# Optimization experiments

Measured on AMD Instinct MI355X. Metric: run time of the kernel, lower is better.

## Reference

```python
import jax, jax.numpy as jnp
import numpy as np

EMB = 1024
HEADS = 16
HEADSIZE = EMB // HEADS


def _layernorm(x, gamma, beta, eps=1e-5):
    # LayerNorm over the last dim (headsize), affine.
    mu = jnp.mean(x, axis=-1, keepdims=True)
    var = jnp.var(x, axis=-1, keepdims=True)
    return (x - mu) * jax.lax.rsqrt(var + eps) * gamma + beta


def setup_inputs() -> dict:
    key = jax.random.key(0)
    ks = jax.random.split(key, 12)
    B, TI, TC = 4, 1024, 1024
    s = 1.0 / np.sqrt(EMB)
    inp = {
        "x": jax.random.normal(ks[0], (B, TI, EMB), dtype=jnp.float32),
        "context": jax.random.normal(ks[1], (B, TC, EMB), dtype=jnp.float32),
        # torch nn.Linear weights are (out, in); y = x @ W.T
        "Wq": jax.random.uniform(ks[2], (EMB, EMB), jnp.float32, -s, s),
        "Wk": jax.random.uniform(ks[3], (EMB, EMB), jnp.float32, -s, s),
        "Wv": jax.random.uniform(ks[4], (EMB, EMB), jnp.float32, -s, s),
        "Wu": jax.random.uniform(ks[5], (EMB, EMB), jnp.float32, -s, s),
        "bu": jax.random.uniform(ks[6], (EMB,), jnp.float32, -s, s),
        "q_gamma": jnp.ones((HEADSIZE,), jnp.float32),
        "q_beta": jnp.zeros((HEADSIZE,), jnp.float32),
        "k_gamma": jnp.ones((HEADSIZE,), jnp.float32),
        "k_beta": jnp.zeros((HEADSIZE,), jnp.float32),
    }
    return inp


def reference(x, context, Wq, Wk, Wv, Wu, bu, q_gamma, q_beta, k_gamma, k_beta):
    B, TI, E = x.shape
    TC = context.shape[1]
    T = TI + TC
    xc = jnp.concatenate([x, context], axis=1)  # [B, T, E]

    q = (x @ Wq.T).reshape(B, TI, HEADS, HEADSIZE)
    k = (xc @ Wk.T).reshape(B, T, HEADS, HEADSIZE)
    v = (xc @ Wv.T).reshape(B, T, HEADS, HEADSIZE)

    # optional QK-LayerNorm over headsize
    q = _layernorm(q, q_gamma, q_beta)
    k = _layernorm(k, k_gamma, k_beta)

    scale = E ** 0.25
    q = q / scale
    k = k / scale

    # scores: [B, H, TI, T]
    dot = jnp.einsum("bihd,bjhd->bhij", q, k)
    attn = jax.nn.softmax(dot, axis=-1)
    out = jnp.einsum("bhij,bjhd->bihd", attn, v).reshape(B, TI, E)
    return out @ Wu.T + bu
```

## Files before the change

kernel.cpp:

```cpp
#include <hip/hip_runtime.h>
#include <cstdint>


typedef unsigned short u16;
typedef __attribute__((ext_vector_type(8))) short bf16x8;
typedef __attribute__((ext_vector_type(4))) float f32x4;
typedef __attribute__((ext_vector_type(4))) unsigned short u16x4;

#define GLDS(gsrc, ldst)                                                              \
  __builtin_amdgcn_global_load_lds(                                                   \
      (const __attribute__((address_space(1))) unsigned int*)(gsrc),                  \
      (__attribute__((address_space(3))) unsigned int*)(ldst), 16, 0, 0)

__device__ __forceinline__ u16 f2bf(float x) {
  unsigned int u = __float_as_uint(x);
  u += 0x7fffu + ((u >> 16) & 1u);
  return (u16)(u >> 16);
}

__device__ __forceinline__ f32x4 mfma16(bf16x8 a, bf16x8 b, f32x4 c) {
  return __builtin_amdgcn_mfma_f32_16x16x32_bf16(a, b, c, 0, 0, 0);
}


__global__ __launch_bounds__(256) void cast_concat(const float* __restrict__ x,
                                                   const float* __restrict__ c,
                                                   u16* __restrict__ o) {
  const int n4 = (8 << 20) / 4;
  for (int i = blockIdx.x * blockDim.x + threadIdx.x; i < n4; i += gridDim.x * blockDim.x) {
    int elem = i * 4;
    int b = elem >> 21;
    int rem = elem & ((1 << 21) - 1);
    int r = rem >> 10;
    int e = rem & 1023;
    const float* src = (r < 1024) ? (x + ((((size_t)(b << 10)) + r) << 10) + e)
                                  : (c + ((((size_t)(b << 10)) + (r - 1024)) << 10) + e);
    float4 v = *(const float4*)src;
    u16x4 ov;
    ov.x = f2bf(v.x); ov.y = f2bf(v.y); ov.z = f2bf(v.z); ov.w = f2bf(v.w);
    *(u16x4*)(o + elem) = ov;
  }
}

__global__ __launch_bounds__(256) void cast_w(const float* __restrict__ w0,
                                              const float* __restrict__ w1,
                                              const float* __restrict__ w2,
                                              const float* __restrict__ w3,
                                              u16* __restrict__ o) {
  const int n4 = (4 << 20) / 4;
  for (int i = blockIdx.x * blockDim.x + threadIdx.x; i < n4; i += gridDim.x * blockDim.x) {
    int elem = i * 4;
    int sel = elem >> 20;
    int loc = elem & ((1 << 20) - 1);
    const float* s = (sel == 0) ? w0 : (sel == 1) ? w1 : (sel == 2) ? w2 : w3;
    float4 v = *(const float4*)(s + loc);
    u16x4 ov;
    ov.x = f2bf(v.x); ov.y = f2bf(v.y); ov.z = f2bf(v.z); ov.w = f2bf(v.w);
    *(u16x4*)(o + elem) = ov;
  }
}


template <int EPI>
__global__ __launch_bounds__(256)
void gemm_bt(const u16* __restrict__ A, const u16* __restrict__ Bw,
             u16* __restrict__ Ob, float* __restrict__ Of,
             const float* __restrict__ P0, const float* __restrict__ P1,
             int M, int N, int K, int rpbo, int rpbi, float oscale) {
  __shared__ alignas(16) u16 lA[128 * 32];
  __shared__ alignas(16) u16 lB[128 * 32];
  const int tid = threadIdx.x;
  const int wv = tid >> 6, l = tid & 63, g = l >> 4, c16 = l & 15;
  const int wr = wv >> 1, wc = wv & 1;
  const int m0 = blockIdx.x * 128, n0 = blockIdx.y * 128;
  const int arow0 = (m0 / rpbo) * rpbi + (m0 % rpbo);

  f32x4 acc[4][4];
  const f32x4 z4 = {0.f, 0.f, 0.f, 0.f};
#pragma unroll
  for (int i = 0; i < 4; ++i)
#pragma unroll
    for (int j = 0; j < 4; ++j) acc[i][j] = z4;

  const int srow = tid >> 2;
  const int scA = (tid & 3) ^ (srow & 3);
  const u16* aSrc = A + (size_t)(arow0 + srow) * K + scA * 8;
  const u16* bSrc = Bw + (size_t)(n0 + srow) * K + scA * 8;
  char* ldA = (char*)lA;
  char* ldB = (char*)lB;
  const int lof = wv * 1024;

  const int ksteps = K >> 5;
  for (int kt = 0; kt < ksteps; ++kt) {
    const int kof = kt << 5;
    GLDS(aSrc + kof, ldA + lof);
    GLDS(aSrc + (size_t)64 * K + kof, ldA + 4096 + lof);
    GLDS(bSrc + kof, ldB + lof);
    GLDS(bSrc + (size_t)64 * K + kof, ldB + 4096 + lof);
    __syncthreads();
    bf16x8 af[4], bfr[4];
#pragma unroll
    for (int mi = 0; mi < 4; ++mi) {
      int row = wr * 64 + mi * 16 + c16;
      af[mi] = *(const bf16x8*)(ldA + row * 64 + ((g * 16) ^ ((row & 3) << 4)));
    }
#pragma unroll
    for (int ni = 0; ni < 4; ++ni) {
      int row = wc * 64 + ni * 16 + c16;
      bfr[ni] = *(const bf16x8*)(ldB + row * 64 + ((g * 16) ^ ((row & 3) << 4)));
    }
#pragma unroll
    for (int mi = 0; mi < 4; ++mi)
#pragma unroll
      for (int ni = 0; ni < 4; ++ni)
        acc[mi][ni] = mfma16(af[mi], bfr[ni], acc[mi][ni]);
    __syncthreads();
  }

  if constexpr (EPI == 2) {
#pragma unroll
    for (int ni = 0; ni < 4; ++ni) {
      int col = n0 + wc * 64 + ni * 16 + c16;
      float bv = P0[col];
#pragma unroll
      for (int mi = 0; mi < 4; ++mi) {
        int row = m0 + wr * 64 + mi * 16 + g * 4;
        float* dst = Of + (size_t)row * N + col;
#pragma unroll
        for (int r = 0; r < 4; ++r) dst[(size_t)r * N] = acc[mi][ni][r] + bv;
      }
    }
  } else if constexpr (EPI == 1) {
#pragma unroll
    for (int ni = 0; ni < 4; ++ni) {
      int col = n0 + wc * 64 + ni * 16 + c16;
      int hh = col >> 6, dd = col & 63;
#pragma unroll
      for (int mi = 0; mi < 4; ++mi) {
        int m = m0 + wr * 64 + mi * 16 + g * 4;
        int bb = m >> 11, tt = m & 2047;
        u16x4 o;
#pragma unroll
        for (int r = 0; r < 4; ++r) o[r] = f2bf(acc[mi][ni][r]);
        *(u16x4*)(Ob + ((size_t)((bb * 16 + hh) * 64 + dd)) * 2048 + tt) = o;
      }
    }
  } else {
#pragma unroll
    for (int mi = 0; mi < 4; ++mi) {
      float sum[4], sq[4];
#pragma unroll
      for (int r = 0; r < 4; ++r) {
        float s = 0.f, q = 0.f;
#pragma unroll
        for (int ni = 0; ni < 4; ++ni) {
          float v = acc[mi][ni][r];
          s += v;
          q += v * v;
        }
#pragma unroll
        for (int msk = 1; msk < 16; msk <<= 1) {
          s += __shfl_xor(s, msk);
          q += __shfl_xor(q, msk);
        }
        sum[r] = s;
        sq[r] = q;
      }
#pragma unroll
      for (int ni = 0; ni < 4; ++ni) {
        int dloc = ni * 16 + c16;
        int colg = n0 + wc * 64 + ni * 16 + c16;
        float gv = P0[dloc], bv = P1[dloc];
#pragma unroll
        for (int r = 0; r < 4; ++r) {
          float mean = sum[r] * (1.f / 64.f);
          float var = sq[r] * (1.f / 64.f) - mean * mean;
          float y = (acc[mi][ni][r] - mean) * rsqrtf(var + 1e-5f) * gv + bv;
          int row = m0 + wr * 64 + mi * 16 + g * 4 + r;
          Ob[(size_t)row * N + colg] = f2bf(y * oscale);
        }
      }
    }
  }
}


__global__ __launch_bounds__(256)
void attn_kernel(const u16* __restrict__ Q, const u16* __restrict__ Kb,
                 const u16* __restrict__ Vt, u16* __restrict__ AO) {
  __shared__ alignas(16) u16 lK[64 * 64];
  __shared__ alignas(16) u16 lV[64 * 64];
  const int tid = threadIdx.x;
  const int wv = tid >> 6, l = tid & 63, g = l >> 4, c16 = l & 15;
  const int b = blockIdx.z, h = blockIdx.y, qt = blockIdx.x;
  const int qrow = (b << 10) + (qt << 6) + (wv << 4) + c16;

  const u16* qp = Q + (size_t)qrow * 1024 + h * 64 + g * 8;
  bf16x8 qf0 = *(const bf16x8*)(qp);
  bf16x8 qf1 = *(const bf16x8*)(qp + 32);

  const f32x4 z4 = {0.f, 0.f, 0.f, 0.f};
  f32x4 acc_o[4];
#pragma unroll
  for (int i = 0; i < 4; ++i) acc_o[i] = z4;
  float m_run = -3.0e38f, l_run = 0.f;

  const u16* Kbase = Kb + (size_t)(b * 2048) * 1024 + (size_t)h * 64;
  const u16* Vbase = Vt + (size_t)((b * 16 + h) * 64) * 2048;
  const int prow = tid >> 3, pch = tid & 7;
  const int sc = pch ^ (prow & 7);
  const int lof = wv * 1024;

  for (int t32 = 0; t32 < 32; ++t32) {
    const int kv0 = t32 << 6;
    GLDS(Kbase + (size_t)(kv0 + prow) * 1024 + sc * 8, (char*)lK + lof);
    GLDS(Kbase + (size_t)(kv0 + prow + 32) * 1024 + sc * 8, (char*)lK + 4096 + lof);
    GLDS(Vbase + (size_t)prow * 2048 + kv0 + sc * 8, (char*)lV + lof);
    GLDS(Vbase + (size_t)(prow + 32) * 2048 + kv0 + sc * 8, (char*)lV + 4096 + lof);
    __syncthreads();

    f32x4 s[4];
#pragma unroll
    for (int nk = 0; nk < 4; ++nk) s[nk] = z4;
#pragma unroll
    for (int nk = 0; nk < 4; ++nk) {
      int row = nk * 16 + c16;
      int swz = (row & 7) << 4;
      bf16x8 ka0 = *(const bf16x8*)((char*)lK + row * 128 + ((g * 16) ^ swz));
      bf16x8 ka1 = *(const bf16x8*)((char*)lK + row * 128 + ((64 + g * 16) ^ swz));
      s[nk] = mfma16(ka0, qf0, s[nk]);
      s[nk] = mfma16(ka1, qf1, s[nk]);
    }

    float tm = -3.0e38f;
#pragma unroll
    for (int nk = 0; nk < 4; ++nk)
#pragma unroll
      for (int r = 0; r < 4; ++r) tm = fmaxf(tm, s[nk][r]);
    tm = fmaxf(tm, __shfl_xor(tm, 16));
    tm = fmaxf(tm, __shfl_xor(tm, 32));
    float mnew = fmaxf(m_run, tm);
    float corr = __expf(m_run - mnew);
    float ts = 0.f;
#pragma unroll
    for (int nk = 0; nk < 4; ++nk)
#pragma unroll
      for (int r = 0; r < 4; ++r) {
        float p = __expf(s[nk][r] - mnew);
        s[nk][r] = p;
        ts += p;
      }
    ts += __shfl_xor(ts, 16);
    ts += __shfl_xor(ts, 32);
    l_run = l_run * corr + ts;
    m_run = mnew;
#pragma unroll
    for (int nd = 0; nd < 4; ++nd) acc_o[nd] *= corr;

    unsigned int pk[4][2];
#pragma unroll
    for (int nk = 0; nk < 4; ++nk) {
      pk[nk][0] = (unsigned int)f2bf(s[nk][0]) | ((unsigned int)f2bf(s[nk][1]) << 16);
      pk[nk][1] = (unsigned int)f2bf(s[nk][2]) | ((unsigned int)f2bf(s[nk][3]) << 16);
    }

#pragma unroll
    for (int c = 0; c < 2; ++c) {
      union {
        unsigned int w[4];
        bf16x8 v;
      } pb;
#pragma unroll
      for (int wj = 0; wj < 4; ++wj) {
        int srcl = ((l & 16) << 1) + ((wj & 2) << 3) + c16;
        unsigned int lo = (unsigned int)__shfl((int)pk[c * 2][wj & 1], srcl);
        unsigned int hi = (unsigned int)__shfl((int)pk[c * 2 + 1][wj & 1], srcl);
        pb.w[wj] = (l & 32) ? hi : lo;
      }
#pragma unroll
      for (int nd = 0; nd < 4; ++nd) {
        int row = nd * 16 + c16;
        int swz = (row & 7) << 4;
        bf16x8 va = *(const bf16x8*)((char*)lV + row * 128 + (((c << 6) + (g << 4)) ^ swz));
        acc_o[nd] = mfma16(va, pb.v, acc_o[nd]);
      }
    }
    __syncthreads();
  }

  float invl = 1.f / l_run;
#pragma unroll
  for (int nd = 0; nd < 4; ++nd) {
    u16x4 o;
#pragma unroll
    for (int r = 0; r < 4; ++r) o[r] = f2bf(acc_o[nd][r] * invl);
    *(u16x4*)(AO + (size_t)qrow * 1024 + h * 64 + nd * 16 + (g << 2)) = o;
  }
}


extern "C" void kernel_launch(void* const* d_in, const int* in_sizes, int n_in,
                              void* d_out, int out_size, void* d_ws, size_t ws_size,
                              hipStream_t stream) {
  const float* x = (const float*)d_in[0];
  const float* ctx = (const float*)d_in[1];
  const float* Wq = (const float*)d_in[2];
  const float* Wk = (const float*)d_in[3];
  const float* Wv = (const float*)d_in[4];
  const float* Wu = (const float*)d_in[5];
  const float* bu = (const float*)d_in[6];
  const float* qg = (const float*)d_in[7];
  const float* qb = (const float*)d_in[8];
  const float* kg = (const float*)d_in[9];
  const float* kb = (const float*)d_in[10];
  float* out = (float*)d_out;

  char* w = (char*)d_ws;
  u16* XCB = (u16*)(w);
  u16* WQB = (u16*)(w + ((size_t)16 << 20));
  u16* WKB = (u16*)(w + ((size_t)18 << 20));
  u16* WVB = (u16*)(w + ((size_t)20 << 20));
  u16* WUB = (u16*)(w + ((size_t)22 << 20));
  u16* QBB = (u16*)(w + ((size_t)24 << 20));
  u16* KBB = (u16*)(w + ((size_t)32 << 20));
  u16* VT = (u16*)(w + ((size_t)48 << 20));
  u16* AO = (u16*)(w + ((size_t)64 << 20));

  const float invs = 0.17677669529663687f;

  cast_concat<<<2048, 256, 0, stream>>>(x, ctx, XCB);
  cast_w<<<1024, 256, 0, stream>>>(Wq, Wk, Wv, Wu, WQB);

  gemm_bt<0><<<dim3(32, 8), 256, 0, stream>>>(XCB, WQB, QBB, nullptr, qg, qb,
                                              4096, 1024, 1024, 1024, 2048, invs);
  gemm_bt<0><<<dim3(64, 8), 256, 0, stream>>>(XCB, WKB, KBB, nullptr, kg, kb,
                                              8192, 1024, 1024, 2048, 2048, invs);
  gemm_bt<1><<<dim3(64, 8), 256, 0, stream>>>(XCB, WVB, VT, nullptr, nullptr, nullptr,
                                              8192, 1024, 1024, 2048, 2048, 1.f);

  attn_kernel<<<dim3(16, 16, 4), 256, 0, stream>>>(QBB, KBB, VT, AO);

  gemm_bt<2><<<dim3(32, 8), 256, 0, stream>>>(AO, WUB, nullptr, out, bu, nullptr,
                                              4096, 1024, 1024, 4096, 4096, 1.f);
}
```

Before: 305.0 us.

## Double-buffer GEMM and attention tiles, switch attention to 32x32 MFMA with lazy rescale

Adds double-buffered LDS staging to the GEMM and attention loops so the next tile's global-to-LDS load is issued before the current tile is computed. The attention kernel is rewritten around 32x32x16 MFMA with 128 query rows per block (half the grid). It folds log2(e) into the Q scale so exp2f can be used, and skips the running-max rescale unless the max grows by more than 8. It also uses s_setprio around the MFMA sections and drops the LDS swizzle in attention. The costs are doubled LDS use, possible bank conflicts from the unswizzled layout, and the lazy rescale relying on bounded exponent growth for numerical safety.

```diff
diff --git a/kernel.cpp b/kernel.cpp
--- a/kernel.cpp
+++ b/kernel.cpp
@@ -5,6 +5,7 @@
 typedef unsigned short u16;
 typedef __attribute__((ext_vector_type(8))) short bf16x8;
 typedef __attribute__((ext_vector_type(4))) float f32x4;
+typedef __attribute__((ext_vector_type(16))) float f32x16;
 typedef __attribute__((ext_vector_type(4))) unsigned short u16x4;
 
 #define GLDS(gsrc, ldst)                                                              \
@@ -20,6 +21,9 @@
 
 __device__ __forceinline__ f32x4 mfma16(bf16x8 a, bf16x8 b, f32x4 c) {
   return __builtin_amdgcn_mfma_f32_16x16x32_bf16(a, b, c, 0, 0, 0);
+}
+__device__ __forceinline__ f32x16 mfma32(bf16x8 a, bf16x8 b, f32x16 c) {
+  return __builtin_amdgcn_mfma_f32_32x32x16_bf16(a, b, c, 0, 0, 0);
 }
 
 
@@ -67,8 +71,8 @@
              u16* __restrict__ Ob, float* __restrict__ Of,
              const float* __restrict__ P0, const float* __restrict__ P1,
              int M, int N, int K, int rpbo, int rpbi, float oscale) {
-  __shared__ alignas(16) u16 lA[128 * 32];
-  __shared__ alignas(16) u16 lB[128 * 32];
+  __shared__ alignas(16) u16 lA[2][128 * 32];
+  __shared__ alignas(16) u16 lB[2][128 * 32];
   const int tid = threadIdx.x;
   const int wv = tid >> 6, l = tid & 63, g = l >> 4, c16 = l & 15;
   const int wr = wv >> 1, wc = wv & 1;
@@ -91,23 +95,33 @@
   const int lof = wv * 1024;
 
   const int ksteps = K >> 5;
+#define STAGE_G(bi, kof)                                   \
+  {                                                        \
+    char* dA = ldA + (bi)*8192 + lof;                      \
+    char* dB = ldB + (bi)*8192 + lof;                      \
+    GLDS(aSrc + (kof), dA);                                \
+    GLDS(aSrc + (size_t)64 * K + (kof), dA + 4096);        \
+    GLDS(bSrc + (kof), dB);                                \
+    GLDS(bSrc + (size_t)64 * K + (kof), dB + 4096);        \
+  }
+
+  STAGE_G(0, 0);
+  __syncthreads();
+  int buf = 0;
   for (int kt = 0; kt < ksteps; ++kt) {
-    const int kof = kt << 5;
-    GLDS(aSrc + kof, ldA + lof);
-    GLDS(aSrc + (size_t)64 * K + kof, ldA + 4096 + lof);
-    GLDS(bSrc + kof, ldB + lof);
-    GLDS(bSrc + (size_t)64 * K + kof, ldB + 4096 + lof);
-    __syncthreads();
+    if (kt + 1 < ksteps) STAGE_G(buf ^ 1, (kt + 1) << 5);
+    const char* bA = ldA + buf * 8192;
+    const char* bB = ldB + buf * 8192;
     bf16x8 af[4], bfr[4];
 #pragma unroll
     for (int mi = 0; mi < 4; ++mi) {
       int row = wr * 64 + mi * 16 + c16;
-      af[mi] = *(const bf16x8*)(ldA + row * 64 + ((g * 16) ^ ((row & 3) << 4)));
+      af[mi] = *(const bf16x8*)(bA + row * 64 + ((g * 16) ^ ((row & 3) << 4)));
     }
 #pragma unroll
     for (int ni = 0; ni < 4; ++ni) {
       int row = wc * 64 + ni * 16 + c16;
-      bfr[ni] = *(const bf16x8*)(ldB + row * 64 + ((g * 16) ^ ((row & 3) << 4)));
+      bfr[ni] = *(const bf16x8*)(bB + row * 64 + ((g * 16) ^ ((row & 3) << 4)));
     }
 #pragma unroll
     for (int mi = 0; mi < 4; ++mi)
@@ -115,7 +129,9 @@
       for (int ni = 0; ni < 4; ++ni)
         acc[mi][ni] = mfma16(af[mi], bfr[ni], acc[mi][ni]);
     __syncthreads();
-  }
+    buf ^= 1;
+  }
+#undef STAGE_G
 
   if constexpr (EPI == 2) {
 #pragma unroll
@@ -188,114 +204,142 @@
 __global__ __launch_bounds__(256)
 void attn_kernel(const u16* __restrict__ Q, const u16* __restrict__ Kb,
                  const u16* __restrict__ Vt, u16* __restrict__ AO) {
-  __shared__ alignas(16) u16 lK[64 * 64];
-  __shared__ alignas(16) u16 lV[64 * 64];
+  __shared__ alignas(16) u16 lK[2][4096];
+  __shared__ alignas(16) u16 lV[2][4096];
   const int tid = threadIdx.x;
-  const int wv = tid >> 6, l = tid & 63, g = l >> 4, c16 = l & 15;
+  const int wv = tid >> 6, l = tid & 63;
+  const int lq = l & 31, hi = l >> 5;
   const int b = blockIdx.z, h = blockIdx.y, qt = blockIdx.x;
-  const int qrow = (b << 10) + (qt << 6) + (wv << 4) + c16;
-
-  const u16* qp = Q + (size_t)qrow * 1024 + h * 64 + g * 8;
-  bf16x8 qf0 = *(const bf16x8*)(qp);
-  bf16x8 qf1 = *(const bf16x8*)(qp + 32);
-
-  const f32x4 z4 = {0.f, 0.f, 0.f, 0.f};
-  f32x4 acc_o[4];
-#pragma unroll
-  for (int i = 0; i < 4; ++i) acc_o[i] = z4;
-  float m_run = -3.0e38f, l_run = 0.f;
-
-  const u16* Kbase = Kb + (size_t)(b * 2048) * 1024 + (size_t)h * 64;
-  const u16* Vbase = Vt + (size_t)((b * 16 + h) * 64) * 2048;
-  const int prow = tid >> 3, pch = tid & 7;
-  const int sc = pch ^ (prow & 7);
-  const int lof = wv * 1024;
-
-  for (int t32 = 0; t32 < 32; ++t32) {
-    const int kv0 = t32 << 6;
-    GLDS(Kbase + (size_t)(kv0 + prow) * 1024 + sc * 8, (char*)lK + lof);
-    GLDS(Kbase + (size_t)(kv0 + prow + 32) * 1024 + sc * 8, (char*)lK + 4096 + lof);
-    GLDS(Vbase + (size_t)prow * 2048 + kv0 + sc * 8, (char*)lV + lof);
-    GLDS(Vbase + (size_t)(prow + 32) * 2048 + kv0 + sc * 8, (char*)lV + 4096 + lof);
+  const int qrow = (b << 10) + (qt << 7) + (wv << 5) + lq;
+
+  const u16* qp = Q + (size_t)qrow * 1024 + h * 64 + hi * 8;
+  bf16x8 qf[4];
+#pragma unroll
+  for (int kk = 0; kk < 4; ++kk) qf[kk] = *(const bf16x8*)(qp + 16 * kk);
+
+  f32x16 acc[2];
+#pragma unroll
+  for (int d0 = 0; d0 < 2; ++d0)
+#pragma unroll
+    for (int i = 0; i < 16; ++i) acc[d0][i] = 0.f;
+  float m_run = -1e30f, l_run = 0.f;
+
+  const u16* Ksrc = Kb + ((size_t)(b * 2048) + l) * 1024 + h * 64 + wv * 8;
+  const u16* Vsrc = Vt + ((size_t)((b * 16 + h) * 64) + l) * 2048 + wv * 8;
+  char* ldK = (char*)lK;
+  char* ldV = (char*)lV;
+
+#define STAGE_KV(bi, kv0)                                  \
+  {                                                        \
+    char* dK = ldK + (bi)*8192 + wv * 1024;                \
+    char* dV = ldV + (bi)*8192 + wv * 1024;                \
+    const u16* ks = Ksrc + (size_t)(kv0) * 1024;           \
+    const u16* vs = Vsrc + (kv0);                          \
+    GLDS(ks, dK);                                          \
+    GLDS(ks + 32, dK + 4096);                              \
+    GLDS(vs, dV);                                          \
+    GLDS(vs + 32, dV + 4096);                              \
+  }
+
+  STAGE_KV(0, 0);
+  __syncthreads();
+  int buf = 0;
+
+  for (int t = 0; t < 32; ++t) {
+    if (t + 1 < 32) STAGE_KV(buf ^ 1, (t + 1) << 6);
+    const char* bK = ldK + buf * 8192;
+    const char* bV = ldV + buf * 8192;
+
+    f32x16 s[2];
+#pragma unroll
+    for (int kvh = 0; kvh < 2; ++kvh)
+#pragma unroll
+      for (int i = 0; i < 16; ++i) s[kvh][i] = 0.f;
+    __builtin_amdgcn_s_setprio(1);
+#pragma unroll
+    for (int kk = 0; kk < 4; ++kk) {
+      const char* kbase = bK + (2 * kk + hi) * 1024;
+      bf16x8 kf0 = *(const bf16x8*)(kbase + lq * 16);
+      bf16x8 kf1 = *(const bf16x8*)(kbase + (32 + lq) * 16);
+      s[0] = mfma32(kf0, qf[kk], s[0]);
+      s[1] = mfma32(kf1, qf[kk], s[1]);
+    }
+    __builtin_amdgcn_s_setprio(0);
+
+    float tm = s[0][0];
+#pragma unroll
+    for (int i = 1; i < 16; ++i) tm = fmaxf(tm, s[0][i]);
+#pragma unroll
+    for (int i = 0; i < 16; ++i) tm = fmaxf(tm, s[1][i]);
+    tm = fmaxf(tm, __shfl_xor(tm, 32));
+    if (!__all(tm <= m_run + 8.f)) {
+      float mnew = fmaxf(m_run, tm);
+      float corr = exp2f(m_run - mnew);
+      l_run *= corr;
+#pragma unroll
+      for (int d0 = 0; d0 < 2; ++d0)
+#pragma unroll
+        for (int i = 0; i < 16; ++i) acc[d0][i] *= corr;
+      m_run = mnew;
+    }
+    float ts = 0.f;
+#pragma unroll
+    for (int kvh = 0; kvh < 2; ++kvh)
+#pragma unroll
+      for (int i = 0; i < 16; ++i) {
+        float p = exp2f(s[kvh][i] - m_run);
+        s[kvh][i] = p;
+        ts += p;
+      }
+    ts += __shfl_xor(ts, 32);
+    l_run += ts;
+
+    unsigned int pk[2][4][2];
+#pragma unroll
+    for (int kvh = 0; kvh < 2; ++kvh)
+#pragma unroll
+      for (int kp = 0; kp < 4; ++kp)
+#pragma unroll
+        for (int tt = 0; tt < 2; ++tt)
+          pk[kvh][kp][tt] = (unsigned)f2bf(s[kvh][4 * kp + 2 * tt]) |
+                            ((unsigned)f2bf(s[kvh][4 * kp + 2 * tt + 1]) << 16);
+
+#pragma unroll
+    for (int kk = 0; kk < 4; ++kk) {
+      const int kvh = kk >> 1, kb = kk & 1;
+      union { unsigned w[4]; bf16x8 v; } bw;
+#pragma unroll
+      for (int tt = 0; tt < 2; ++tt) {
+        unsigned A0 = pk[kvh][2 * kb][tt];
+        unsigned A1 = pk[kvh][2 * kb + 1][tt];
+        unsigned S = (unsigned)__shfl_xor((int)(hi ? A0 : A1), 32);
+        bw.w[tt] = hi ? S : A0;
+        bw.w[2 + tt] = hi ? A1 : S;
+      }
+      const char* vbase = bV + (2 * kk + hi) * 1024;
+      bf16x8 vf0 = *(const bf16x8*)(vbase + lq * 16);
+      bf16x8 vf1 = *(const bf16x8*)(vbase + (32 + lq) * 16);
+      __builtin_amdgcn_s_setprio(1);
+      acc[0] = mfma32(vf0, bw.v, acc[0]);
+      acc[1] = mfma32(vf1, bw.v, acc[1]);
+      __builtin_amdgcn_s_setprio(0);
+    }
     __syncthreads();
-
-    f32x4 s[4];
-#pragma unroll
-    for (int nk = 0; nk < 4; ++nk) s[nk] = z4;
-#pragma unroll
-    for (int nk = 0; nk < 4; ++nk) {
-      int row = nk * 16 + c16;
-      int swz = (row & 7) << 4;
-      bf16x8 ka0 = *(const bf16x8*)((char*)lK + row * 128 + ((g * 16) ^ swz));
-      bf16x8 ka1 = *(const bf16x8*)((char*)lK + row * 128 + ((64 + g * 16) ^ swz));
-      s[nk] = mfma16(ka0, qf0, s[nk]);
-      s[nk] = mfma16(ka1, qf1, s[nk]);
-    }
-
-    float tm = -3.0e38f;
-#pragma unroll
-    for (int nk = 0; nk < 4; ++nk)
-#pragma unroll
-      for (int r = 0; r < 4; ++r) tm = fmaxf(tm, s[nk][r]);
-    tm = fmaxf(tm, __shfl_xor(tm, 16));
-    tm = fmaxf(tm, __shfl_xor(tm, 32));
-    float mnew = fmaxf(m_run, tm);
-    float corr = __expf(m_run - mnew);
-    float ts = 0.f;
-#pragma unroll
-    for (int nk = 0; nk < 4; ++nk)
-#pragma unroll
-      for (int r = 0; r < 4; ++r) {
-        float p = __expf(s[nk][r] - mnew);
-        s[nk][r] = p;
-        ts += p;
-      }
-    ts += __shfl_xor(ts, 16);
-    ts += __shfl_xor(ts, 32);
-    l_run = l_run * corr + ts;
-    m_run = mnew;
-#pragma unroll
-    for (int nd = 0; nd < 4; ++nd) acc_o[nd] *= corr;
-
-    unsigned int pk[4][2];
-#pragma unroll
-    for (int nk = 0; nk < 4; ++nk) {
-      pk[nk][0] = (unsigned int)f2bf(s[nk][0]) | ((unsigned int)f2bf(s[nk][1]) << 16);
-      pk[nk][1] = (unsigned int)f2bf(s[nk][2]) | ((unsigned int)f2bf(s[nk][3]) << 16);
-    }
-
-#pragma unroll
-    for (int c = 0; c < 2; ++c) {
-      union {
-        unsigned int w[4];
-        bf16x8 v;
-      } pb;
-#pragma unroll
-      for (int wj = 0; wj < 4; ++wj) {
-        int srcl = ((l & 16) << 1) + ((wj & 2) << 3) + c16;
-        unsigned int lo = (unsigned int)__shfl((int)pk[c * 2][wj & 1], srcl);
-        unsigned int hi = (unsigned int)__shfl((int)pk[c * 2 + 1][wj & 1], srcl);
-        pb.w[wj] = (l & 32) ? hi : lo;
-      }
-#pragma unroll
-      for (int nd = 0; nd < 4; ++nd) {
-        int row = nd * 16 + c16;
-        int swz = (row & 7) << 4;
-        bf16x8 va = *(const bf16x8*)((char*)lV + row * 128 + (((c << 6) + (g << 4)) ^ swz));
-        acc_o[nd] = mfma16(va, pb.v, acc_o[nd]);
-      }
-    }
-    __syncthreads();
-  }
+    buf ^= 1;
+  }
+#undef STAGE_KV
 
   float invl = 1.f / l_run;
 #pragma unroll
-  for (int nd = 0; nd < 4; ++nd) {
-    u16x4 o;
-#pragma unroll
-    for (int r = 0; r < 4; ++r) o[r] = f2bf(acc_o[nd][r] * invl);
-    *(u16x4*)(AO + (size_t)qrow * 1024 + h * 64 + nd * 16 + (g << 2)) = o;
-  }
+  for (int d0 = 0; d0 < 2; ++d0)
+#pragma unroll
+    for (int rg = 0; rg < 4; ++rg) {
+      u16x4 o;
+#pragma unroll
+      for (int rr = 0; rr < 4; ++rr) o[rr] = f2bf(acc[d0][4 * rg + rr] * invl);
+      int d = 32 * d0 + 8 * rg + 4 * hi;
+      *(u16x4*)(AO + (size_t)qrow * 1024 + h * 64 + d) = o;
+    }
 }
 
 
@@ -327,18 +371,19 @@
   u16* AO = (u16*)(w + ((size_t)64 << 20));
 
   const float invs = 0.17677669529663687f;
+  const float invs_l2e = invs * 1.44269504088896f;
 
   cast_concat<<<2048, 256, 0, stream>>>(x, ctx, XCB);
   cast_w<<<1024, 256, 0, stream>>>(Wq, Wk, Wv, Wu, WQB);
 
   gemm_bt<0><<<dim3(32, 8), 256, 0, stream>>>(XCB, WQB, QBB, nullptr, qg, qb,
-                                              4096, 1024, 1024, 1024, 2048, invs);
+                                              4096, 1024, 1024, 1024, 2048, invs_l2e);
   gemm_bt<0><<<dim3(64, 8), 256, 0, stream>>>(XCB, WKB, KBB, nullptr, kg, kb,
                                               8192, 1024, 1024, 2048, 2048, invs);
   gemm_bt<1><<<dim3(64, 8), 256, 0, stream>>>(XCB, WVB, VT, nullptr, nullptr, nullptr,
                                               8192, 1024, 1024, 2048, 2048, 1.f);
 
-  attn_kernel<<<dim3(16, 16, 4), 256, 0, stream>>>(QBB, KBB, VT, AO);
+  attn_kernel<<<dim3(8, 16, 4), 256, 0, stream>>>(QBB, KBB, VT, AO);
 
   gemm_bt<2><<<dim3(32, 8), 256, 0, stream>>>(AO, WUB, nullptr, out, bu, nullptr,
                                               4096, 1024, 1024, 4096, 4096, 1.f);
```

New measurement: 302.6 us. No clear change (-0.8%).
